# Kernel tuning notes

Measured on AMD Instinct MI355X. Metric: run time of the kernel, lower is better.

The kernel has to match this reference:

```python
import jax, jax.numpy as jnp
import numpy as np

Nn, Nt, Np, Ne = 100000, 30000, 400000, 1000000
IN_NODE, IN_NET, IN_PIN, IN_EDGE = 16, 8, 8, 4
H, HP, HE, L, T = 64, 16, 8, 3, 4
LOG2 = 0.6931471805599453  # ShiftedSoftplus shift


def _lrelu(x):
    return jax.nn.leaky_relu(x, 0.01)


def _ssp(x):  # DGL ShiftedSoftplus: softplus(x) - log(2)
    return jax.nn.softplus(x) - LOG2


def _forward(in_node_feat, in_net_feat, in_pin_feat, in_edge_feat,
             pins_src, pins_dst, near_src, near_dst,
             node_lin_W, node_lin_b, net_lin_W, net_lin_b,
             pin_lin_W, pin_lin_b, edge_lin_W, edge_lin_b,
             geom_W, geom_b, pins_W, pins_b,
             cf_node_W, cf_node_b, cf_e1_W, cf_e1_b, cf_e2_W, cf_e2_b,
             cf_out_W, cf_out_b, sage_pool_W, sage_pool_b,
             sage_self_W, sage_neigh_W, sage_bias,
             out1_W, out1_b, out2_W, out2_b, out3_W, out3_b,
             outn1_W, outn1_b, outn2_W, outn2_b, outn3_W, outn3_b):
    node_feat = _lrelu(in_node_feat @ node_lin_W + node_lin_b)   # [Nn,H]
    net_feat = _lrelu(in_net_feat @ net_lin_W + net_lin_b)       # [Nt,H]
    pin_feat = _lrelu(in_pin_feat @ pin_lin_W + pin_lin_b)       # [Np,HP]
    edge_feat = _lrelu(in_edge_feat @ edge_lin_W + edge_lin_b)   # [Ne,HE]

    # static degree norms for GraphConv(norm='both') on 'pins' (node->net)
    ones_p = jnp.ones((Np,), jnp.float32)
    deg_out = jax.ops.segment_sum(ones_p, pins_src, num_segments=Nn)
    deg_in = jax.ops.segment_sum(ones_p, pins_dst, num_segments=Nt)
    src_norm = jnp.clip(deg_out, 1.0, None) ** -0.5
    dst_norm = jnp.clip(deg_in, 1.0, None) ** -0.5

    for i in range(L):
        # --- 'pins' GraphConv (node -> net), norm='both' ---
        msg = (node_feat * src_norm[:, None])[pins_src]                 # [Np,H]
        agg = jax.ops.segment_sum(msg, pins_dst, num_segments=Nt)      # [Nt,H]
        net_out = (agg * dst_norm[:, None]) @ pins_W[i] + pins_b[i]

        # --- 'pinned' CFConv (net -> node), reverse pins, edge feats = pin_feat ---
        hv = net_feat @ cf_node_W[i] + cf_node_b[i]                    # [Nt,H]
        he = _ssp(pin_feat @ cf_e1_W[i] + cf_e1_b[i])
        he = _ssp(he @ cf_e2_W[i] + cf_e2_b[i])                        # [Np,H]
        m = hv[pins_dst] * he                                          # src of 'pinned' = pins_dst
        h_cf = jax.ops.segment_sum(m, pins_src, num_segments=Nn)       # dst of 'pinned' = pins_src
        node_cf = _ssp(h_cf @ cf_out_W[i] + cf_out_b[i])

        # --- 'near' SAGEConv(pool) with sigmoid edge weights ---
        ew = jax.nn.sigmoid(edge_feat @ geom_W[i] + geom_b[i])         # [Ne,1]
        hp = jax.nn.relu(node_feat @ sage_pool_W[i] + sage_pool_b[i])  # [Nn,H]
        m2 = hp[near_src] * ew                                         # [Ne,H], nonnegative
        h_neigh = jax.ops.segment_max(m2, near_dst, num_segments=Nn)
        h_neigh = jnp.maximum(h_neigh, 0.0)  # zero-degree nodes -> 0 (msgs are >= 0)
        node_sage = node_feat @ sage_self_W[i] + h_neigh @ sage_neigh_W[i] + sage_bias[i]

        # hetero max-aggregation over edge types hitting dst 'node'
        node_feat = _lrelu(jnp.maximum(node_cf, node_sage))
        net_feat = _lrelu(net_out)

    h = _lrelu(jnp.concatenate([in_node_feat, node_feat], axis=-1) @ out1_W + out1_b)
    h = _lrelu(h @ out2_W + out2_b)
    node_pred = jax.nn.sigmoid(h @ out3_W + out3_b)
    g = _lrelu(jnp.concatenate([in_net_feat, net_feat], axis=-1) @ outn1_W + outn1_b)
    g = _lrelu(g @ outn2_W + outn2_b)
    net_pred = jax.nn.sigmoid(g @ outn3_W + outn3_b)
    return node_pred, net_pred


def setup_inputs() -> dict:
    key = jax.random.key(0)
    ks = iter(jax.random.split(key, 80))

    def nrm(shape, scale=0.05):
        return jax.random.normal(next(ks), shape, jnp.float32) * scale

    inp = {}
    inp['in_node_feat'] = nrm((Nn, IN_NODE), 1.0)
    inp['in_net_feat'] = nrm((Nt, IN_NET), 1.0)
    inp['in_pin_feat'] = nrm((Np, IN_PIN), 1.0)
    inp['in_edge_feat'] = nrm((Ne, IN_EDGE), 1.0)
    inp['pins_src'] = jax.random.randint(next(ks), (Np,), 0, Nn)
    inp['pins_dst'] = jax.random.randint(next(ks), (Np,), 0, Nt)
    inp['near_src'] = jax.random.randint(next(ks), (Ne,), 0, Nn)
    inp['near_dst'] = jax.random.randint(next(ks), (Ne,), 0, Nn)
    inp['node_lin_W'] = nrm((IN_NODE, H)); inp['node_lin_b'] = nrm((H,))
    inp['net_lin_W'] = nrm((IN_NET, H)); inp['net_lin_b'] = nrm((H,))
    inp['pin_lin_W'] = nrm((IN_PIN, HP)); inp['pin_lin_b'] = nrm((HP,))
    inp['edge_lin_W'] = nrm((IN_EDGE, HE)); inp['edge_lin_b'] = nrm((HE,))
    inp['geom_W'] = nrm((L, HE, 1)); inp['geom_b'] = nrm((L, 1))
    inp['pins_W'] = nrm((L, H, H)); inp['pins_b'] = nrm((L, H))
    inp['cf_node_W'] = nrm((L, H, H)); inp['cf_node_b'] = nrm((L, H))
    inp['cf_e1_W'] = nrm((L, HP, H)); inp['cf_e1_b'] = nrm((L, H))
    inp['cf_e2_W'] = nrm((L, H, H)); inp['cf_e2_b'] = nrm((L, H))
    inp['cf_out_W'] = nrm((L, H, H)); inp['cf_out_b'] = nrm((L, H))
    inp['sage_pool_W'] = nrm((L, H, H)); inp['sage_pool_b'] = nrm((L, H))
    inp['sage_self_W'] = nrm((L, H, H))
    inp['sage_neigh_W'] = nrm((L, H, H))
    inp['sage_bias'] = nrm((L, H))
    inp['out1_W'] = nrm((IN_NODE + H, H)); inp['out1_b'] = nrm((H,))
    inp['out2_W'] = nrm((H, H)); inp['out2_b'] = nrm((H,))
    inp['out3_W'] = nrm((H, T)); inp['out3_b'] = nrm((T,))
    inp['outn1_W'] = nrm((IN_NET + H, H)); inp['outn1_b'] = nrm((H,))
    inp['outn2_W'] = nrm((H, H)); inp['outn2_b'] = nrm((H,))
    inp['outn3_W'] = nrm((H, 1)); inp['outn3_b'] = nrm((1,))
    return inp


def reference(in_node_feat, in_net_feat, in_pin_feat, in_edge_feat,
              pins_src, pins_dst, near_src, near_dst,
              node_lin_W, node_lin_b, net_lin_W, net_lin_b,
              pin_lin_W, pin_lin_b, edge_lin_W, edge_lin_b,
              geom_W, geom_b, pins_W, pins_b,
              cf_node_W, cf_node_b, cf_e1_W, cf_e1_b, cf_e2_W, cf_e2_b,
              cf_out_W, cf_out_b, sage_pool_W, sage_pool_b,
              sage_self_W, sage_neigh_W, sage_bias,
              out1_W, out1_b, out2_W, out2_b, out3_W, out3_b,
              outn1_W, outn1_b, outn2_W, outn2_b, outn3_W, outn3_b):
    return _forward(in_node_feat, in_net_feat, in_pin_feat, in_edge_feat,
                    pins_src, pins_dst, near_src, near_dst,
                    node_lin_W, node_lin_b, net_lin_W, net_lin_b,
                    pin_lin_W, pin_lin_b, edge_lin_W, edge_lin_b,
                    geom_W, geom_b, pins_W, pins_b,
                    cf_node_W, cf_node_b, cf_e1_W, cf_e1_b, cf_e2_W, cf_e2_b,
                    cf_out_W, cf_out_b, sage_pool_W, sage_pool_b,
                    sage_self_W, sage_neigh_W, sage_bias,
                    out1_W, out1_b, out2_W, out2_b, out3_W, out3_b,
                    outn1_W, outn1_b, outn2_W, outn2_b, outn3_W, outn3_b)
```

## Files before the change

kernel.cpp:

```cpp
#include <hip/hip_runtime.h>
#include <hip/hip_bf16.h>

#define DEV __device__ __forceinline__

DEV float lrelu_(float x){ return x > 0.f ? x : 0.01f * x; }
DEV float ssp_(float x){ return fmaxf(x, 0.f) + __logf(1.f + __expf(-fabsf(x))) - 0.69314718055994530942f; }
DEV float sigm_(float x){ return 1.f / (1.f + __expf(-x)); }

DEV unsigned short f2bf(float x){
    unsigned int u = __float_as_uint(x);
    unsigned int r = (u + 0x7FFFu + ((u >> 16) & 1u)) >> 16;
    return (unsigned short)r;
}
DEV float bf2f(unsigned short s){ return __uint_as_float((unsigned int)s << 16); }
DEV ushort4 pack4(float4 v){
    ushort4 u; u.x = f2bf(v.x); u.y = f2bf(v.y); u.z = f2bf(v.z); u.w = f2bf(v.w); return u;
}

DEV void fma44(float (&acc)[4][4], const float4 (&xa)[4], const float4 (&wa)[4])
{
    #pragma unroll
    for (int kk = 0; kk < 4; kk++) {
        #pragma unroll
        for (int i = 0; i < 4; i++) {
            float x = ((const float*)&xa[i])[kk];
            #pragma unroll
            for (int j = 0; j < 4; j++)
                acc[i][j] += x * ((const float*)&wa[kk])[j];
        }
    }
}

typedef short s8v __attribute__((ext_vector_type(8)));
typedef float f4v __attribute__((ext_vector_type(4)));

template<int K, int ACT, bool OUTBF>
__global__ __launch_bounds__(256) void gemm64_kernel(const float* __restrict__ X,
                                                     const float* __restrict__ W,
                                                     const float* __restrict__ B,
                                                     void* __restrict__ Yv, int nrows)
{
    constexpr int XS = K + 4;
    constexpr int KQ = K / 4;
    __shared__ float Ws[K * 64];
    __shared__ float bs[64];
    __shared__ float Xs[64 * XS];
    for (int i = threadIdx.x; i < K * 64; i += 256) Ws[i] = W[i];
    if (threadIdx.x < 64) bs[threadIdx.x] = B[threadIdx.x];
    const int tr = threadIdx.x >> 4, tc = threadIdx.x & 15;
    const int r0 = tr * 4, c0 = tc * 4;
    for (int base = blockIdx.x * 64; base < nrows; base += gridDim.x * 64) {
        __syncthreads();
        for (int i = threadIdx.x; i < 64 * KQ; i += 256) {
            int row = i / KQ, kq = (i % KQ) * 4;
            int g = base + row;
            float4 v = make_float4(0.f, 0.f, 0.f, 0.f);
            if (g < nrows) v = *(const float4*)&X[(size_t)g * K + kq];
            *(float4*)&Xs[row * XS + kq] = v;
        }
        __syncthreads();
        float acc[4][4];
        #pragma unroll
        for (int i = 0; i < 4; i++)
            #pragma unroll
            for (int j = 0; j < 4; j++) acc[i][j] = bs[c0 + j];
        #pragma unroll 4
        for (int kq = 0; kq < K; kq += 4) {
            float4 xa[4], wa[4];
            #pragma unroll
            for (int i = 0; i < 4; i++) xa[i] = *(const float4*)&Xs[(r0 + i) * XS + kq];
            #pragma unroll
            for (int j = 0; j < 4; j++) wa[j] = *(const float4*)&Ws[(kq + j) * 64 + c0];
            fma44(acc, xa, wa);
        }
        #pragma unroll
        for (int i = 0; i < 4; i++) {
            int g = base + r0 + i;
            if (g < nrows) {
                float4 o;
                float* op = (float*)&o;
                #pragma unroll
                for (int j = 0; j < 4; j++) {
                    float a = acc[i][j];
                    if (ACT == 1) a = lrelu_(a);
                    else if (ACT == 2) a = fmaxf(a, 0.f);
                    op[j] = a;
                }
                if (OUTBF) *(ushort4*)&((unsigned short*)Yv)[(size_t)g * 64 + c0] = pack4(o);
                else       *(float4*)&((float*)Yv)[(size_t)g * 64 + c0] = o;
            }
        }
    }
}

template<int ACT, bool INBF, bool OUTBF>
__global__ __launch_bounds__(256) void mfma_gemm_kernel(const void* __restrict__ Xv,
                                                        const float* __restrict__ W,
                                                        const float* __restrict__ B,
                                                        void* __restrict__ Yv, int nrows)
{
    __shared__ __align__(16) unsigned short WT[64 * 72];
    __shared__ __align__(16) unsigned short Axs[64 * 72];
    __shared__ float bs[64];
    for (int i = threadIdx.x; i < 4096; i += 256) {
        int k = i >> 6, nn = i & 63;
        WT[nn * 72 + k] = f2bf(W[i]);
    }
    if (threadIdx.x < 64) bs[threadIdx.x] = B[threadIdx.x];
    const int lane = threadIdx.x & 63, wv = threadIdx.x >> 6;
    const int l15 = lane & 15, quad = lane >> 4;
    const int arow = 16 * wv + l15;
    const int koff = quad * 8;
    for (int base = blockIdx.x * 64; base < nrows; base += gridDim.x * 64) {
        __syncthreads();
        {
            int row = threadIdx.x >> 2, kq = (threadIdx.x & 3) * 16;
            int g = base + row;
            if (INBF) {
                const unsigned short* Xb = (const unsigned short*)Xv;
                uint4 v0 = make_uint4(0,0,0,0), v1 = v0;
                if (g < nrows) {
                    v0 = *(const uint4*)&Xb[(size_t)g * 64 + kq];
                    v1 = *(const uint4*)&Xb[(size_t)g * 64 + kq + 8];
                }
                *(uint4*)&Axs[row * 72 + kq] = v0;
                *(uint4*)&Axs[row * 72 + kq + 8] = v1;
            } else {
                const float* Xf = (const float*)Xv;
                #pragma unroll
                for (int m = 0; m < 4; m++) {
                    float4 v = make_float4(0,0,0,0);
                    if (g < nrows) v = *(const float4*)&Xf[(size_t)g * 64 + kq + m * 4];
                    *(ushort4*)&Axs[row * 72 + kq + m * 4] = pack4(v);
                }
            }
        }
        __syncthreads();
        f4v acc[4];
        #pragma unroll
        for (int t = 0; t < 4; t++) acc[t] = (f4v){0.f,0.f,0.f,0.f};
        s8v a0 = *(const s8v*)&Axs[arow * 72 + koff];
        s8v a1 = *(const s8v*)&Axs[arow * 72 + 32 + koff];
        #pragma unroll
        for (int t = 0; t < 4; t++) {
            int nn = t * 16 + l15;
            s8v b0 = *(const s8v*)&WT[nn * 72 + koff];
            s8v b1 = *(const s8v*)&WT[nn * 72 + 32 + koff];
            acc[t] = __builtin_amdgcn_mfma_f32_16x16x32_bf16(a0, b0, acc[t], 0, 0, 0);
            acc[t] = __builtin_amdgcn_mfma_f32_16x16x32_bf16(a1, b1, acc[t], 0, 0, 0);
        }
        const int mrow = 16 * wv + quad * 4;
        #pragma unroll
        for (int t = 0; t < 4; t++) {
            int col = t * 16 + l15;
            float b = bs[col];
            #pragma unroll
            for (int r = 0; r < 4; r++) {
                int g = base + mrow + r;
                if (g < nrows) {
                    float a = acc[t][r] + b;
                    if (ACT == 1) a = lrelu_(a);
                    else if (ACT == 2) a = fmaxf(a, 0.f);
                    if (OUTBF) ((unsigned short*)Yv)[(size_t)g * 64 + col] = f2bf(a);
                    else       ((float*)Yv)[(size_t)g * 64 + col] = a;
                }
            }
        }
    }
}

__global__ __launch_bounds__(256) void mfma_combine_kernel(const unsigned short* __restrict__ cfb,
                                                           const unsigned short* __restrict__ nfb,
                                                           const unsigned short* __restrict__ ngb,
                                                           const float* __restrict__ Wc, const float* __restrict__ cB,
                                                           const float* __restrict__ sW, const float* __restrict__ nW,
                                                           const float* __restrict__ sB,
                                                           unsigned short* __restrict__ outb, int n)
{
    __shared__ __align__(16) unsigned short WcT[64 * 72], WsT[64 * 72], WnT[64 * 72];
    __shared__ __align__(16) unsigned short Ac[32 * 72], As[32 * 72], An[32 * 72];
    __shared__ float bc[64], bsg[64];
    for (int i = threadIdx.x; i < 4096; i += 256) {
        int k = i >> 6, nn = i & 63;
        WcT[nn * 72 + k] = f2bf(Wc[i]);
        WsT[nn * 72 + k] = f2bf(sW[i]);
        WnT[nn * 72 + k] = f2bf(nW[i]);
    }
    if (threadIdx.x < 64) { bc[threadIdx.x] = cB[threadIdx.x]; bsg[threadIdx.x] = sB[threadIdx.x]; }
    const int lane = threadIdx.x & 63, wv = threadIdx.x >> 6;
    const int l15 = lane & 15, quad = lane >> 4;
    const int arow = (wv & 1) * 16 + l15;
    const int ct0 = (wv >> 1) * 2;
    const int koff = quad * 8;
    for (int base = blockIdx.x * 32; base < n; base += gridDim.x * 32) {
        __syncthreads();
        {
            int row = threadIdx.x >> 3, kq = (threadIdx.x & 7) * 8;
            int g = base + row;
            uint4 vc = make_uint4(0,0,0,0), vf = vc, vg = vc;
            if (g < n) {
                vc = *(const uint4*)&cfb[(size_t)g * 64 + kq];
                vf = *(const uint4*)&nfb[(size_t)g * 64 + kq];
                vg = *(const uint4*)&ngb[(size_t)g * 64 + kq];
            }
            *(uint4*)&Ac[row * 72 + kq] = vc;
            *(uint4*)&As[row * 72 + kq] = vf;
            *(uint4*)&An[row * 72 + kq] = vg;
        }
        __syncthreads();
        f4v accC[2], accS[2];
        #pragma unroll
        for (int t = 0; t < 2; t++) { accC[t] = (f4v){0.f,0.f,0.f,0.f}; accS[t] = (f4v){0.f,0.f,0.f,0.f}; }
        s8v ac0 = *(const s8v*)&Ac[arow * 72 + koff];
        s8v ac1 = *(const s8v*)&Ac[arow * 72 + 32 + koff];
        s8v as0 = *(const s8v*)&As[arow * 72 + koff];
        s8v as1 = *(const s8v*)&As[arow * 72 + 32 + koff];
        s8v an0 = *(const s8v*)&An[arow * 72 + koff];
        s8v an1 = *(const s8v*)&An[arow * 72 + 32 + koff];
        #pragma unroll
        for (int t = 0; t < 2; t++) {
            int nn = (ct0 + t) * 16 + l15;
            s8v wc0 = *(const s8v*)&WcT[nn * 72 + koff];
            s8v wc1 = *(const s8v*)&WcT[nn * 72 + 32 + koff];
            accC[t] = __builtin_amdgcn_mfma_f32_16x16x32_bf16(ac0, wc0, accC[t], 0, 0, 0);
            accC[t] = __builtin_amdgcn_mfma_f32_16x16x32_bf16(ac1, wc1, accC[t], 0, 0, 0);
            s8v ws0 = *(const s8v*)&WsT[nn * 72 + koff];
            s8v ws1 = *(const s8v*)&WsT[nn * 72 + 32 + koff];
            accS[t] = __builtin_amdgcn_mfma_f32_16x16x32_bf16(as0, ws0, accS[t], 0, 0, 0);
            accS[t] = __builtin_amdgcn_mfma_f32_16x16x32_bf16(as1, ws1, accS[t], 0, 0, 0);
            s8v wn0 = *(const s8v*)&WnT[nn * 72 + koff];
            s8v wn1 = *(const s8v*)&WnT[nn * 72 + 32 + koff];
            accS[t] = __builtin_amdgcn_mfma_f32_16x16x32_bf16(an0, wn0, accS[t], 0, 0, 0);
            accS[t] = __builtin_amdgcn_mfma_f32_16x16x32_bf16(an1, wn1, accS[t], 0, 0, 0);
        }
        const int mrow = (wv & 1) * 16 + quad * 4;
        #pragma unroll
        for (int t = 0; t < 2; t++) {
            int col = (ct0 + t) * 16 + l15;
            float bcv = bc[col], bsv = bsg[col];
            #pragma unroll
            for (int r = 0; r < 4; r++) {
                int g = base + mrow + r;
                if (g < n)
                    outb[(size_t)g * 64 + col] = f2bf(lrelu_(fmaxf(ssp_(accC[t][r] + bcv), accS[t][r] + bsv)));
            }
        }
    }
}

template<int K, int C, int ACT, bool OUTBF>
__global__ __launch_bounds__(256) void lin_kernel(const float* __restrict__ X,
                                                  const float* __restrict__ W,
                                                  const float* __restrict__ B,
                                                  void* __restrict__ Yv, int nrows)
{
    constexpr int ROWS = 256 / C;
    __shared__ float Ws[K * C];
    __shared__ float bs[C];
    __shared__ float Xs[ROWS * K];
    for (int i = threadIdx.x; i < K * C; i += 256) Ws[i] = W[i];
    if (threadIdx.x < C) bs[threadIdx.x] = B[threadIdx.x];
    __syncthreads();
    const int r = threadIdx.x / C, c = threadIdx.x % C;
    for (int base = blockIdx.x * ROWS; base < nrows; base += gridDim.x * ROWS) {
        __syncthreads();
        for (int i = threadIdx.x; i < ROWS * K; i += 256) {
            int rr = base + i / K;
            Xs[i] = (rr < nrows) ? X[(size_t)rr * K + i % K] : 0.f;
        }
        __syncthreads();
        int row = base + r;
        if (row < nrows) {
            float acc = bs[c];
            #pragma unroll
            for (int k = 0; k < K; k++) acc += Xs[r * K + k] * Ws[k * C + c];
            if (ACT == 1) acc = lrelu_(acc);
            else if (ACT == 2) acc = fmaxf(acc, 0.f);
            if (OUTBF) ((unsigned short*)Yv)[(size_t)row * C + c] = f2bf(acc);
            else       ((float*)Yv)[(size_t)row * C + c] = acc;
        }
    }
}

__global__ __launch_bounds__(256) void deg_kernel(const int* __restrict__ src, const int* __restrict__ dst,
                                                  int* __restrict__ cnt_src, int* __restrict__ cnt_dst, int np)
{
    int p = blockIdx.x * 256 + threadIdx.x;
    if (p < np) { atomicAdd(&cnt_src[src[p]], 1); atomicAdd(&cnt_dst[dst[p]], 1); }
}

__global__ __launch_bounds__(256) void norm_out_kernel(const int* __restrict__ cnt, float* __restrict__ out, int n)
{
    int i = blockIdx.x * 256 + threadIdx.x;
    if (i < n) {
        int v = cnt[i]; if (v < 1) v = 1;
        out[i] = rsqrtf((float)v);
    }
}

__global__ __launch_bounds__(256) void csr_count_kernel(const int* __restrict__ key, int* __restrict__ cnt, int ne)
{
    int e = blockIdx.x * 256 + threadIdx.x;
    if (e < ne) atomicAdd(&cnt[key[e]], 1);
}

__global__ __launch_bounds__(256) void scan_block_sum_kernel(const int* __restrict__ cnt, int* __restrict__ bsum, int n)
{
    __shared__ int sh[256];
    int i = blockIdx.x * 256 + threadIdx.x;
    sh[threadIdx.x] = (i < n) ? cnt[i] : 0;
    __syncthreads();
    for (int s = 128; s > 0; s >>= 1) {
        if (threadIdx.x < s) sh[threadIdx.x] += sh[threadIdx.x + s];
        __syncthreads();
    }
    if (threadIdx.x == 0) bsum[blockIdx.x] = sh[0];
}

__global__ __launch_bounds__(512) void scan_bsum_kernel(int* __restrict__ bsum, int nb, int* __restrict__ total_out)
{
    __shared__ int sh[512];
    int i = threadIdx.x;
    int v = (i < nb) ? bsum[i] : 0;
    sh[i] = v;
    __syncthreads();
    for (int s = 1; s < 512; s <<= 1) {
        int add = (i >= s) ? sh[i - s] : 0;
        __syncthreads();
        sh[i] += add;
        __syncthreads();
    }
    if (i < nb) bsum[i] = sh[i] - v;
    if (i == nb - 1) *total_out = sh[i];
}

__global__ __launch_bounds__(256) void scan_final_kernel(const int* __restrict__ cnt, const int* __restrict__ bsum,
                                                         int* __restrict__ row_start, int* __restrict__ nxt, int n)
{
    __shared__ int sh[256];
    int i = blockIdx.x * 256 + threadIdx.x;
    int v = (i < n) ? cnt[i] : 0;
    sh[threadIdx.x] = v;
    __syncthreads();
    for (int s = 1; s < 256; s <<= 1) {
        int add = (threadIdx.x >= s) ? sh[threadIdx.x - s] : 0;
        __syncthreads();
        sh[threadIdx.x] += add;
        __syncthreads();
    }
    if (i < n) {
        int excl = sh[threadIdx.x] - v + bsum[blockIdx.x];
        row_start[i] = excl;
        nxt[i] = excl;
    }
}

__global__ __launch_bounds__(256) void csr_fill_kernel(const int* __restrict__ key, int* __restrict__ nxt,
                                                       int* __restrict__ eidx, int ne, int nrows)
{
    const int color = blockIdx.x & 7;
    const int bid = blockIdx.x >> 3;
    const int nblk = gridDim.x >> 3;
    const int lo = (int)(((long long)nrows * color) >> 3);
    const int hi = (int)(((long long)nrows * (color + 1)) >> 3);
    for (int e = bid * 256 + threadIdx.x; e < ne; e += nblk * 256) {
        int k = key[e];
        if (k >= lo && k < hi) {
            int slot = atomicAdd(&nxt[k], 1);
            eidx[slot] = e;
        }
    }
}

__global__ __launch_bounds__(256) void pin_permute_kernel(const int* __restrict__ seidx,
                                                          const unsigned short* __restrict__ pinb,
                                                          const int* __restrict__ pdst,
                                                          unsigned short* __restrict__ pinb_s,
                                                          int* __restrict__ pdst_s, int np)
{
    int slot = blockIdx.x * 256 + threadIdx.x;
    if (slot < np) {
        int p = seidx[slot];
        uint4 a = *(const uint4*)&pinb[(size_t)p * 16];
        uint4 b = *(const uint4*)&pinb[(size_t)p * 16 + 8];
        *(uint4*)&pinb_s[(size_t)slot * 16] = a;
        *(uint4*)&pinb_s[(size_t)slot * 16 + 8] = b;
        pdst_s[slot] = pdst[p];
    }
}

__global__ __launch_bounds__(256) void pins_meta_permute_kernel(const int* __restrict__ peidx,
                                                                const int* __restrict__ psrc,
                                                                const float* __restrict__ snorm,
                                                                int* __restrict__ psrc_s,
                                                                float* __restrict__ snorm_s, int np)
{
    int slot = blockIdx.x * 256 + threadIdx.x;
    if (slot < np) {
        int s = psrc[peidx[slot]];
        psrc_s[slot] = s;
        snorm_s[slot] = snorm[s];
    }
}

__global__ __launch_bounds__(256) void near_meta_permute_kernel(const int* __restrict__ eidx,
                                                                const int* __restrict__ esrc,
                                                                int* __restrict__ esrc_s, int ne)
{
    int slot = blockIdx.x * 256 + threadIdx.x;
    if (slot < ne) esrc_s[slot] = esrc[eidx[slot]];
}

__global__ __launch_bounds__(256) void edge_ew_kernel(const float* __restrict__ in_edge,
                                                      const float* __restrict__ elW, const float* __restrict__ elb,
                                                      const float* __restrict__ gW, const float* __restrict__ gb,
                                                      float* __restrict__ ew3, int ne)
{
    __shared__ float W[32], B[8], G[24], Gb[3];
    if (threadIdx.x < 32) W[threadIdx.x] = elW[threadIdx.x];
    if (threadIdx.x < 8)  B[threadIdx.x] = elb[threadIdx.x];
    if (threadIdx.x < 24) G[threadIdx.x] = gW[threadIdx.x];
    if (threadIdx.x < 3)  Gb[threadIdx.x] = gb[threadIdx.x];
    __syncthreads();
    for (int e = blockIdx.x * 256 + threadIdx.x; e < ne; e += gridDim.x * 256) {
        float4 x = *(const float4*)&in_edge[(size_t)e * 4];
        float ef[8];
        #pragma unroll
        for (int j = 0; j < 8; j++)
            ef[j] = lrelu_(B[j] + x.x * W[j] + x.y * W[8 + j] + x.z * W[16 + j] + x.w * W[24 + j]);
        #pragma unroll
        for (int i = 0; i < 3; i++) {
            float a = Gb[i];
            #pragma unroll
            for (int j = 0; j < 8; j++) a += ef[j] * G[i * 8 + j];
            ew3[(size_t)i * ne + e] = sigm_(a);
        }
    }
}

__global__ __launch_bounds__(256) void pins_gather_kernel(const unsigned short* __restrict__ nfb,
                                                          const float* __restrict__ dnorm,
                                                          const int* __restrict__ psrc_s,
                                                          const float* __restrict__ snorm_s,
                                                          const int* __restrict__ prow,
                                                          unsigned short* __restrict__ aggb, int nt)
{
    __shared__ int sS[4][64];
    __shared__ float sN[4][64];
    const int lane = threadIdx.x & 63, wv = threadIdx.x >> 6;
    for (int d = blockIdx.x * 4 + wv; d < nt; d += gridDim.x * 4) {
        int rs = prow[d], re = prow[d + 1];
        float acc = 0.f;
        for (int cbase = rs; cbase < re; cbase += 64) {
            int cnt = re - cbase; if (cnt > 64) cnt = 64;
            if (lane < cnt) {
                sS[wv][lane] = psrc_s[cbase + lane];
                sN[wv][lane] = snorm_s[cbase + lane];
            }
            int k = 0;
            for (; k + 7 < cnt; k += 8) {
                float v[8];
                #pragma unroll
                for (int j = 0; j < 8; j++)
                    v[j] = bf2f(nfb[(size_t)sS[wv][k + j] * 64 + lane]) * sN[wv][k + j];
                acc += ((v[0] + v[1]) + (v[2] + v[3])) + ((v[4] + v[5]) + (v[6] + v[7]));
            }
            for (; k + 3 < cnt; k += 4) {
                float v0 = bf2f(nfb[(size_t)sS[wv][k]   * 64 + lane]) * sN[wv][k];
                float v1 = bf2f(nfb[(size_t)sS[wv][k+1] * 64 + lane]) * sN[wv][k+1];
                float v2 = bf2f(nfb[(size_t)sS[wv][k+2] * 64 + lane]) * sN[wv][k+2];
                float v3 = bf2f(nfb[(size_t)sS[wv][k+3] * 64 + lane]) * sN[wv][k+3];
                acc += (v0 + v1) + (v2 + v3);
            }
            for (; k < cnt; k++)
                acc += bf2f(nfb[(size_t)sS[wv][k] * 64 + lane]) * sN[wv][k];
        }
        aggb[(size_t)d * 64 + lane] = f2bf(acc * dnorm[d]);
    }
}

__global__ __launch_bounds__(256) void cf_pin6_kernel(const unsigned short* __restrict__ pinb,
                                                      const float* __restrict__ W1, const float* __restrict__ B1,
                                                      const float* __restrict__ W2, const float* __restrict__ B2,
                                                      unsigned short* __restrict__ HEb, int np)
{
    __shared__ __align__(16) unsigned short W1T[64 * 40];
    __shared__ __align__(16) unsigned short W2T[64 * 72];
    __shared__ __align__(16) unsigned short PFb[64 * 40];
    __shared__ __align__(16) unsigned short T1s[64 * 72];
    __shared__ float bs1[64], bs2[64];
    for (int i = threadIdx.x; i < 64 * 32; i += 256) {
        int n = i & 63, k = i >> 6;
        W1T[n * 40 + k] = (k < 16) ? f2bf(W1[k * 64 + n]) : (unsigned short)0;
    }
    for (int i = threadIdx.x; i < 4096; i += 256) {
        int k = i >> 6, n = i & 63;
        W2T[n * 72 + k] = f2bf(W2[i]);
    }
    if (threadIdx.x < 64) { bs1[threadIdx.x] = B1[threadIdx.x]; bs2[threadIdx.x] = B2[threadIdx.x]; }
    const int lane = threadIdx.x & 63, wv = threadIdx.x >> 6;
    const int l15 = lane & 15, quad = lane >> 4;
    const int arow = 16 * wv + l15;
    const int koff = quad * 8;
    const int mrow = 16 * wv + quad * 4;
    for (int base = blockIdx.x * 64; base < np; base += gridDim.x * 64) {
        __syncthreads();
        {
            int row = threadIdx.x >> 2, q = threadIdx.x & 3;
            int p = base + row;
            uint2 v = make_uint2(0, 0);
            if (p < np) v = *(const uint2*)&pinb[(size_t)p * 16 + q * 4];
            *(uint2*)&PFb[row * 40 + q * 4] = v;
            if (q < 2)
                *(uint4*)&PFb[row * 40 + 16 + q * 8] = make_uint4(0,0,0,0);
        }
        __syncthreads();
        {
            f4v acc1[4];
            #pragma unroll
            for (int t = 0; t < 4; t++) acc1[t] = (f4v){0.f,0.f,0.f,0.f};
            s8v a = *(const s8v*)&PFb[arow * 40 + koff];
            #pragma unroll
            for (int t = 0; t < 4; t++) {
                int n = t * 16 + l15;
                s8v b = *(const s8v*)&W1T[n * 40 + koff];
                acc1[t] = __builtin_amdgcn_mfma_f32_16x16x32_bf16(a, b, acc1[t], 0, 0, 0);
            }
            #pragma unroll
            for (int t = 0; t < 4; t++) {
                int col = t * 16 + l15;
                float b = bs1[col];
                #pragma unroll
                for (int r = 0; r < 4; r++)
                    T1s[(mrow + r) * 72 + col] = f2bf(ssp_(acc1[t][r] + b));
            }
        }
        __syncthreads();
        {
            f4v acc4[4];
            #pragma unroll
            for (int t = 0; t < 4; t++) acc4[t] = (f4v){0.f, 0.f, 0.f, 0.f};
            s8v a0 = *(const s8v*)&T1s[arow * 72 + koff];
            s8v a1 = *(const s8v*)&T1s[arow * 72 + 32 + koff];
            #pragma unroll
            for (int t = 0; t < 4; t++) {
                int n = t * 16 + l15;
                s8v b0 = *(const s8v*)&W2T[n * 72 + koff];
                s8v b1 = *(const s8v*)&W2T[n * 72 + 32 + koff];
                acc4[t] = __builtin_amdgcn_mfma_f32_16x16x32_bf16(a0, b0, acc4[t], 0, 0, 0);
                acc4[t] = __builtin_amdgcn_mfma_f32_16x16x32_bf16(a1, b1, acc4[t], 0, 0, 0);
            }
            __syncthreads();
            #pragma unroll
            for (int t = 0; t < 4; t++) {
                int col = t * 16 + l15;
                float b = bs2[col];
                #pragma unroll
                for (int r = 0; r < 4; r++)
                    T1s[(mrow + r) * 72 + col] = f2bf(ssp_(acc4[t][r] + b));
            }
        }
        __syncthreads();
        {
            int row = threadIdx.x >> 2, kq = (threadIdx.x & 3) * 16;
            int p = base + row;
            if (p < np) {
                *(uint4*)&HEb[(size_t)p * 64 + kq]     = *(const uint4*)&T1s[row * 72 + kq];
                *(uint4*)&HEb[(size_t)p * 64 + kq + 8] = *(const uint4*)&T1s[row * 72 + kq + 8];
            }
        }
    }
}

__global__ __launch_bounds__(256) void cf_gather_kernel(const unsigned short* __restrict__ HEb,
                                                        const unsigned short* __restrict__ hvb,
                                                        const int* __restrict__ pdst_s,
                                                        const int* __restrict__ srow,
                                                        unsigned short* __restrict__ cfb, int nn)
{
    __shared__ int sD[4][64];
    const int lane = threadIdx.x & 63, wv = threadIdx.x >> 6;
    for (int d = blockIdx.x * 4 + wv; d < nn; d += gridDim.x * 4) {
        int rs = srow[d], re = srow[d + 1];
        float acc = 0.f;
        for (int cbase = rs; cbase < re; cbase += 64) {
            int cnt = re - cbase; if (cnt > 64) cnt = 64;
            if (lane < cnt) {
                sD[wv][lane] = pdst_s[cbase + lane];
            }
            int k = 0;
            for (; k + 3 < cnt; k += 4) {
                float he[4], hv[4];
                #pragma unroll
                for (int j = 0; j < 4; j++) {
                    he[j] = bf2f(HEb[(size_t)(cbase + k + j) * 64 + lane]);
                    hv[j] = bf2f(hvb[(size_t)sD[wv][k + j] * 64 + lane]);
                }
                acc += (he[0] * hv[0] + he[1] * hv[1]) + (he[2] * hv[2] + he[3] * hv[3]);
            }
            for (; k < cnt; k++) {
                acc += bf2f(HEb[(size_t)(cbase + k) * 64 + lane]) * bf2f(hvb[(size_t)sD[wv][k] * 64 + lane]);
            }
        }
        cfb[(size_t)d * 64 + lane] = f2bf(acc);
    }
}

__global__ __launch_bounds__(256) void sage_gather_kernel(const unsigned short* __restrict__ hpb,
                                                          const float* __restrict__ ew,
                                                          const int* __restrict__ esrc_s,
                                                          const int* __restrict__ row_start,
                                                          const int* __restrict__ eidx,
                                                          unsigned short* __restrict__ ngb, int nn)
{
    __shared__ int sS[4][64];
    __shared__ float sWt[4][64];
    const int lane = threadIdx.x & 63, wv = threadIdx.x >> 6;
    for (int d = blockIdx.x * 4 + wv; d < nn; d += gridDim.x * 4) {
        int rs = row_start[d], re = row_start[d + 1];
        float acc = 0.f;
        for (int cbase = rs; cbase < re; cbase += 64) {
            int cnt = re - cbase; if (cnt > 64) cnt = 64;
            if (lane < cnt) {
                sS[wv][lane] = esrc_s[cbase + lane];
                sWt[wv][lane] = ew[eidx[cbase + lane]];
            }
            int k = 0;
            for (; k + 7 < cnt; k += 8) {
                float v[8];
                #pragma unroll
                for (int j = 0; j < 8; j++)
                    v[j] = bf2f(hpb[(size_t)sS[wv][k + j] * 64 + lane]) * sWt[wv][k + j];
                float m0 = fmaxf(fmaxf(v[0], v[1]), fmaxf(v[2], v[3]));
                float m1 = fmaxf(fmaxf(v[4], v[5]), fmaxf(v[6], v[7]));
                acc = fmaxf(acc, fmaxf(m0, m1));
            }
            for (; k + 3 < cnt; k += 4) {
                float v0 = bf2f(hpb[(size_t)sS[wv][k]   * 64 + lane]) * sWt[wv][k];
                float v1 = bf2f(hpb[(size_t)sS[wv][k+1] * 64 + lane]) * sWt[wv][k+1];
                float v2 = bf2f(hpb[(size_t)sS[wv][k+2] * 64 + lane]) * sWt[wv][k+2];
                float v3 = bf2f(hpb[(size_t)sS[wv][k+3] * 64 + lane]) * sWt[wv][k+3];
                acc = fmaxf(acc, fmaxf(fmaxf(v0, v1), fmaxf(v2, v3)));
            }
            for (; k < cnt; k++)
                acc = fmaxf(acc, bf2f(hpb[(size_t)sS[wv][k] * 64 + lane]) * sWt[wv][k]);
        }
        ngb[(size_t)d * 64 + lane] = f2bf(acc);
    }
}

__global__ __launch_bounds__(256) void node_head_mfma_kernel(const float* __restrict__ in_node,
                                                             const unsigned short* __restrict__ nfb,
                                                             const float* __restrict__ W1, const float* __restrict__ B1,
                                                             const float* __restrict__ W2, const float* __restrict__ B2,
                                                             const float* __restrict__ W3, const float* __restrict__ B3,
                                                             float* __restrict__ out, int n)
{
    __shared__ __align__(16) unsigned short W1T[64 * 104];
    __shared__ __align__(16) unsigned short W2T[64 * 72];
    __shared__ __align__(16) unsigned short W3T[16 * 72];
    __shared__ __align__(16) unsigned short Xs[64 * 104];
    __shared__ __align__(16) unsigned short H1[64 * 72];
    __shared__ float bs1[64], bs2[64], bs3[4];
    for (int i = threadIdx.x; i < 64 * 96; i += 256) {
        int k = i >> 6, nn = i & 63;
        W1T[nn * 104 + k] = (k < 80) ? f2bf(W1[k * 64 + nn]) : (unsigned short)0;
    }
    for (int i = threadIdx.x; i < 4096; i += 256) {
        int k = i >> 6, nn = i & 63;
        W2T[nn * 72 + k] = f2bf(W2[i]);
    }
    for (int i = threadIdx.x; i < 1024; i += 256) {
        int k = i >> 4, c = i & 15;
        W3T[c * 72 + k] = (c < 4) ? f2bf(W3[k * 4 + c]) : (unsigned short)0;
    }
    if (threadIdx.x < 64) { bs1[threadIdx.x] = B1[threadIdx.x]; bs2[threadIdx.x] = B2[threadIdx.x]; }
    if (threadIdx.x < 4) bs3[threadIdx.x] = B3[threadIdx.x];
    const int lane = threadIdx.x & 63, wv = threadIdx.x >> 6;
    const int l15 = lane & 15, quad = lane >> 4;
    const int arow = 16 * wv + l15;
    const int koff = quad * 8;
    const int mrow = 16 * wv + quad * 4;
    unsigned short* H2 = Xs;
    for (int base = blockIdx.x * 64; base < n; base += gridDim.x * 64) {
        __syncthreads();
        {
            int row = threadIdx.x >> 2, q = threadIdx.x & 3;
            int g = base + row;
            float4 v = make_float4(0,0,0,0);
            if (g < n) v = *(const float4*)&in_node[(size_t)g * 16 + q * 4];
            *(ushort4*)&Xs[row * 104 + q * 4] = pack4(v);
            uint4 u0 = make_uint4(0,0,0,0), u1 = u0;
            if (g < n) {
                u0 = *(const uint4*)&nfb[(size_t)g * 64 + q * 16];
                u1 = *(const uint4*)&nfb[(size_t)g * 64 + q * 16 + 8];
            }
            *(uint4*)&Xs[row * 104 + 16 + q * 16] = u0;
            *(uint4*)&Xs[row * 104 + 16 + q * 16 + 8] = u1;
            ushort4 z; z.x = 0; z.y = 0; z.z = 0; z.w = 0;
            *(ushort4*)&Xs[row * 104 + 80 + q * 4] = z;
        }
        __syncthreads();
        {
            f4v acc[4];
            #pragma unroll
            for (int t = 0; t < 4; t++) acc[t] = (f4v){0.f,0.f,0.f,0.f};
            s8v a0 = *(const s8v*)&Xs[arow * 104 + koff];
            s8v a1 = *(const s8v*)&Xs[arow * 104 + 32 + koff];
            s8v a2 = *(const s8v*)&Xs[arow * 104 + 64 + koff];
            #pragma unroll
            for (int t = 0; t < 4; t++) {
                int nn = t * 16 + l15;
                s8v b0 = *(const s8v*)&W1T[nn * 104 + koff];
                s8v b1 = *(const s8v*)&W1T[nn * 104 + 32 + koff];
                s8v b2 = *(const s8v*)&W1T[nn * 104 + 64 + koff];
                acc[t] = __builtin_amdgcn_mfma_f32_16x16x32_bf16(a0, b0, acc[t], 0, 0, 0);
                acc[t] = __builtin_amdgcn_mfma_f32_16x16x32_bf16(a1, b1, acc[t], 0, 0, 0);
                acc[t] = __builtin_amdgcn_mfma_f32_16x16x32_bf16(a2, b2, acc[t], 0, 0, 0);
            }
            #pragma unroll
            for (int t = 0; t < 4; t++) {
                int col = t * 16 + l15;
                float b = bs1[col];
                #pragma unroll
                for (int r = 0; r < 4; r++)
                    H1[(mrow + r) * 72 + col] = f2bf(lrelu_(acc[t][r] + b));
            }
        }
        __syncthreads();
        {
            f4v acc[4];
            #pragma unroll
            for (int t = 0; t < 4; t++) acc[t] = (f4v){0.f,0.f,0.f,0.f};
            s8v a0 = *(const s8v*)&H1[arow * 72 + koff];
            s8v a1 = *(const s8v*)&H1[arow * 72 + 32 + koff];
            #pragma unroll
            for (int t = 0; t < 4; t++) {
                int nn = t * 16 + l15;
                s8v b0 = *(const s8v*)&W2T[nn * 72 + koff];
                s8v b1 = *(const s8v*)&W2T[nn * 72 + 32 + koff];
                acc[t] = __builtin_amdgcn_mfma_f32_16x16x32_bf16(a0, b0, acc[t], 0, 0, 0);
                acc[t] = __builtin_amdgcn_mfma_f32_16x16x32_bf16(a1, b1, acc[t], 0, 0, 0);
            }
            __syncthreads();
            #pragma unroll
            for (int t = 0; t < 4; t++) {
                int col = t * 16 + l15;
                float b = bs2[col];
                #pragma unroll
                for (int r = 0; r < 4; r++)
                    H2[(mrow + r) * 72 + col] = f2bf(lrelu_(acc[t][r] + b));
            }
        }
        __syncthreads();
        {
            f4v acc = (f4v){0.f,0.f,0.f,0.f};
            s8v a0 = *(const s8v*)&H2[arow * 72 + koff];
            s8v a1 = *(const s8v*)&H2[arow * 72 + 32 + koff];
            s8v b0 = *(const s8v*)&W3T[l15 * 72 + koff];
            s8v b1 = *(const s8v*)&W3T[l15 * 72 + 32 + koff];
            acc = __builtin_amdgcn_mfma_f32_16x16x32_bf16(a0, b0, acc, 0, 0, 0);
            acc = __builtin_amdgcn_mfma_f32_16x16x32_bf16(a1, b1, acc, 0, 0, 0);
            if (l15 < 4) {
                float b = bs3[l15];
                #pragma unroll
                for (int r = 0; r < 4; r++) {
                    int g = base + mrow + r;
                    if (g < n) out[(size_t)g * 4 + l15] = sigm_(acc[r] + b);
                }
            }
        }
    }
}

__global__ __launch_bounds__(256) void net_head_mfma_kernel(const float* __restrict__ in_net, const float* __restrict__ tf,
                                                            const float* __restrict__ W1, const float* __restrict__ B1,
                                                            const float* __restrict__ W2, const float* __restrict__ B2,
                                                            const float* __restrict__ W3, const float* __restrict__ B3,
                                                            float* __restrict__ out, int n)
{
    __shared__ __align__(16) unsigned short W1T[64 * 104];
    __shared__ __align__(16) unsigned short W2T[64 * 72];
    __shared__ __align__(16) unsigned short W3T[16 * 72];
    __shared__ __align__(16) unsigned short Xs[64 * 104];
    __shared__ __align__(16) unsigned short H1[64 * 72];
    __shared__ float bs1[64], bs2[64], bs3[1];
    for (int i = threadIdx.x; i < 64 * 96; i += 256) {
        int k = i >> 6, nn = i & 63;
        W1T[nn * 104 + k] = (k < 72) ? f2bf(W1[k * 64 + nn]) : (unsigned short)0;
    }
    for (int i = threadIdx.x; i < 4096; i += 256) {
        int k = i >> 6, nn = i & 63;
        W2T[nn * 72 + k] = f2bf(W2[i]);
    }
    for (int i = threadIdx.x; i < 1024; i += 256) {
        int k = i >> 4, c = i & 15;
        W3T[c * 72 + k] = (c == 0) ? f2bf(W3[k]) : (unsigned short)0;
    }
    if (threadIdx.x < 64) { bs1[threadIdx.x] = B1[threadIdx.x]; bs2[threadIdx.x] = B2[threadIdx.x]; }
    if (threadIdx.x == 0) bs3[0] = B3[0];
    const int lane = threadIdx.x & 63, wv = threadIdx.x >> 6;
    const int l15 = lane & 15, quad = lane >> 4;
    const int arow = 16 * wv + l15;
    const int koff = quad * 8;
    const int mrow = 16 * wv + quad * 4;
    unsigned short* H2 = Xs;
    for (int base = blockIdx.x * 64; base < n; base += gridDim.x * 64) {
        __syncthreads();
        {
            int row = threadIdx.x >> 2, q = threadIdx.x & 3;
            int g = base + row;
            if (q < 2) {
                float4 v = make_float4(0,0,0,0);
                if (g < n) v = *(const float4*)&in_net[(size_t)g * 8 + q * 4];
                *(ushort4*)&Xs[row * 104 + q * 4] = pack4(v);
            }
            #pragma unroll
            for (int m = 0; m < 4; m++) {
                float4 v = make_float4(0,0,0,0);
                if (g < n) v = *(const float4*)&tf[(size_t)g * 64 + q * 16 + m * 4];
                *(ushort4*)&Xs[row * 104 + 8 + q * 16 + m * 4] = pack4(v);
            }
            if (q < 3) {
                ushort4 z; z.x = 0; z.y = 0; z.z = 0; z.w = 0;
                *(ushort4*)&Xs[row * 104 + 72 + q * 8] = z;
                *(ushort4*)&Xs[row * 104 + 72 + q * 8 + 4] = z;
            }
        }
        __syncthreads();
        {
            f4v acc[4];
            #pragma unroll
            for (int t = 0; t < 4; t++) acc[t] = (f4v){0.f,0.f,0.f,0.f};
            s8v a0 = *(const s8v*)&Xs[arow * 104 + koff];
            s8v a1 = *(const s8v*)&Xs[arow * 104 + 32 + koff];
            s8v a2 = *(const s8v*)&Xs[arow * 104 + 64 + koff];
            #pragma unroll
            for (int t = 0; t < 4; t++) {
                int nn = t * 16 + l15;
                s8v b0 = *(const s8v*)&W1T[nn * 104 + koff];
                s8v b1 = *(const s8v*)&W1T[nn * 104 + 32 + koff];
                s8v b2 = *(const s8v*)&W1T[nn * 104 + 64 + koff];
                acc[t] = __builtin_amdgcn_mfma_f32_16x16x32_bf16(a0, b0, acc[t], 0, 0, 0);
                acc[t] = __builtin_amdgcn_mfma_f32_16x16x32_bf16(a1, b1, acc[t], 0, 0, 0);
                acc[t] = __builtin_amdgcn_mfma_f32_16x16x32_bf16(a2, b2, acc[t], 0, 0, 0);
            }
            #pragma unroll
            for (int t = 0; t < 4; t++) {
                int col = t * 16 + l15;
                float b = bs1[col];
                #pragma unroll
                for (int r = 0; r < 4; r++)
                    H1[(mrow + r) * 72 + col] = f2bf(lrelu_(acc[t][r] + b));
            }
        }
        __syncthreads();
        {
            f4v acc[4];
            #pragma unroll
            for (int t = 0; t < 4; t++) acc[t] = (f4v){0.f,0.f,0.f,0.f};
            s8v a0 = *(const s8v*)&H1[arow * 72 + koff];
            s8v a1 = *(const s8v*)&H1[arow * 72 + 32 + koff];
            #pragma unroll
            for (int t = 0; t < 4; t++) {
                int nn = t * 16 + l15;
                s8v b0 = *(const s8v*)&W2T[nn * 72 + koff];
                s8v b1 = *(const s8v*)&W2T[nn * 72 + 32 + koff];
                acc[t] = __builtin_amdgcn_mfma_f32_16x16x32_bf16(a0, b0, acc[t], 0, 0, 0);
                acc[t] = __builtin_amdgcn_mfma_f32_16x16x32_bf16(a1, b1, acc[t], 0, 0, 0);
            }
            __syncthreads();
            #pragma unroll
            for (int t = 0; t < 4; t++) {
                int col = t * 16 + l15;
                float b = bs2[col];
                #pragma unroll
                for (int r = 0; r < 4; r++)
                    H2[(mrow + r) * 72 + col] = f2bf(lrelu_(acc[t][r] + b));
            }
        }
        __syncthreads();
        {
            f4v acc = (f4v){0.f,0.f,0.f,0.f};
            s8v a0 = *(const s8v*)&H2[arow * 72 + koff];
            s8v a1 = *(const s8v*)&H2[arow * 72 + 32 + koff];
            s8v b0 = *(const s8v*)&W3T[l15 * 72 + koff];
            s8v b1 = *(const s8v*)&W3T[l15 * 72 + 32 + koff];
            acc = __builtin_amdgcn_mfma_f32_16x16x32_bf16(a0, b0, acc, 0, 0, 0);
            acc = __builtin_amdgcn_mfma_f32_16x16x32_bf16(a1, b1, acc, 0, 0, 0);
            if (l15 == 0) {
                float b = bs3[0];
                #pragma unroll
                for (int r = 0; r < 4; r++) {
                    int g = base + mrow + r;
                    if (g < n) out[g] = sigm_(acc[r] + b);
                }
            }
        }
    }
}

extern "C" void kernel_launch(void* const* d_in, const int* in_sizes, int n_in,
                              void* d_out, int out_size, void* d_ws, size_t ws_size,
                              hipStream_t stream)
{
    (void)in_sizes; (void)n_in; (void)out_size; (void)ws_size;
    constexpr int Nn = 100000, Nt = 30000, Np = 400000, Ne = 1000000;
    constexpr int H = 64, L = 3, T = 4;

    auto fpt = [&](int i){ return (const float*)d_in[i]; };
    auto ipt = [&](int i){ return (const int*)d_in[i]; };

    const float* in_node = fpt(0);
    const float* in_net  = fpt(1);
    const float* in_pin  = fpt(2);
    const float* in_edge = fpt(3);
    const int* psrc = ipt(4);
    const int* pdst = ipt(5);
    const int* esrc = ipt(6);
    const int* edst = ipt(7);

    float* ws = (float*)d_ws;
    size_t o = 0;
    auto alloc = [&](size_t nel){ float* p = ws + o; o += nel; return p; };
    unsigned short* node_a = (unsigned short*)alloc((size_t)Nn * 32);
    unsigned short* node_b = (unsigned short*)alloc((size_t)Nn * 32);
    unsigned short* aggb   = (unsigned short*)alloc((size_t)Nt * 32);
    unsigned short* hvb    = (unsigned short*)alloc((size_t)Nt * 32);
    unsigned short* hpb    = (unsigned short*)alloc((size_t)Nn * 32);
    unsigned short* ngb    = (unsigned short*)alloc((size_t)Nn * 32);
    unsigned short* HEb    = (unsigned short*)alloc((size_t)Np * 32);
    unsigned short* cfb    = (unsigned short*)alloc((size_t)Nn * 32);
    float* net_a  = alloc((size_t)Nt * H);
    float* net_b  = alloc((size_t)Nt * H);
    unsigned short* pinb   = (unsigned short*)alloc((size_t)Np * 8);
    unsigned short* pinb_s = (unsigned short*)alloc((size_t)Np * 8);
    float* ew3    = alloc((size_t)3 * Ne);
    float* snorm  = alloc((size_t)Nn);
    float* dnorm  = alloc((size_t)Nt);
    int* cnt       = (int*)alloc((size_t)Nn);
    int* ecnt      = (int*)alloc((size_t)Nn);
    int* row_start = (int*)alloc((size_t)Nn + 1);
    int* nxt       = (int*)alloc((size_t)Nn);
    int* eidx      = (int*)alloc((size_t)Ne);
    int* bsum      = (int*)alloc((size_t)512);
    int* pcnt      = (int*)alloc((size_t)Nt);
    int* prow      = (int*)alloc((size_t)Nt + 1);
    int* pnxt      = (int*)alloc((size_t)Nt);
    int* peidx     = (int*)alloc((size_t)Np);
    int* pbsum     = (int*)alloc((size_t)256);
    int* srow      = (int*)alloc((size_t)Nn + 1);
    int* seidx     = (int*)alloc((size_t)Np);
    int* pdst_s    = (int*)alloc((size_t)Np);
    int* psrc_s    = (int*)alloc((size_t)Np);
    float* snorm_s = alloc((size_t)Np);
    int* esrc_s    = (int*)alloc((size_t)Ne);

    constexpr int NB  = (Nn + 255) / 256;
    constexpr int NB2 = (Nt + 255) / 256;

    hipMemsetAsync(cnt, 0, (size_t)Nn * 4, stream);
    hipMemsetAsync(pcnt, 0, (size_t)Nt * 4, stream);
    deg_kernel<<<(Np + 255) / 256, 256, 0, stream>>>(psrc, pdst, cnt, pcnt, Np);
    norm_out_kernel<<<(Nn + 255) / 256, 256, 0, stream>>>(cnt, snorm, Nn);
    norm_out_kernel<<<(Nt + 255) / 256, 256, 0, stream>>>(pcnt, dnorm, Nt);

    hipMemsetAsync(ecnt, 0, (size_t)Nn * 4, stream);
    csr_count_kernel<<<(Ne + 255) / 256, 256, 0, stream>>>(edst, ecnt, Ne);
    scan_block_sum_kernel<<<NB, 256, 0, stream>>>(ecnt, bsum, Nn);
    scan_bsum_kernel<<<1, 512, 0, stream>>>(bsum, NB, row_start + Nn);
    scan_final_kernel<<<NB, 256, 0, stream>>>(ecnt, bsum, row_start, nxt, Nn);
    csr_fill_kernel<<<2048, 256, 0, stream>>>(edst, nxt, eidx, Ne, Nn);
    near_meta_permute_kernel<<<(Ne + 255) / 256, 256, 0, stream>>>(eidx, esrc, esrc_s, Ne);

    scan_block_sum_kernel<<<NB2, 256, 0, stream>>>(pcnt, pbsum, Nt);
    scan_bsum_kernel<<<1, 512, 0, stream>>>(pbsum, NB2, prow + Nt);
    scan_final_kernel<<<NB2, 256, 0, stream>>>(pcnt, pbsum, prow, pnxt, Nt);
    csr_fill_kernel<<<1024, 256, 0, stream>>>(pdst, pnxt, peidx, Np, Nt);
    pins_meta_permute_kernel<<<(Np + 255) / 256, 256, 0, stream>>>(peidx, psrc, snorm, psrc_s, snorm_s, Np);

    scan_block_sum_kernel<<<NB, 256, 0, stream>>>(cnt, bsum, Nn);
    scan_bsum_kernel<<<1, 512, 0, stream>>>(bsum, NB, srow + Nn);
    scan_final_kernel<<<NB, 256, 0, stream>>>(cnt, bsum, srow, nxt, Nn);
    csr_fill_kernel<<<1024, 256, 0, stream>>>(psrc, nxt, seidx, Np, Nn);

    gemm64_kernel<16, 1, true><<<1024, 256, 0, stream>>>(in_node, fpt(8),  fpt(9),  node_a, Nn);
    gemm64_kernel< 8, 1, false><<<469, 256, 0, stream>>>(in_net,  fpt(10), fpt(11), net_a,  Nt);
    lin_kernel<8, 16, 1, true><<<1024, 256, 0, stream>>>(in_pin, fpt(12), fpt(13), pinb, Np);
    edge_ew_kernel<<<2048, 256, 0, stream>>>(in_edge, fpt(14), fpt(15), fpt(16), fpt(17), ew3, Ne);

    pin_permute_kernel<<<(Np + 255) / 256, 256, 0, stream>>>(seidx, pinb, pdst, pinb_s, pdst_s, Np);

    unsigned short* ncur = node_a; unsigned short* nnew = node_b;
    float* tcur = net_a;  float* tnew = net_b;

    for (int i = 0; i < L; i++) {
        pins_gather_kernel<<<(Nt + 3) / 4, 256, 0, stream>>>(ncur, dnorm, psrc_s, snorm_s, prow, aggb, Nt);
        mfma_gemm_kernel<1, true, false><<<469, 256, 0, stream>>>(aggb, fpt(18) + (size_t)i * 4096, fpt(19) + (size_t)i * 64, tnew, Nt);

        mfma_gemm_kernel<0, false, true><<<469, 256, 0, stream>>>(tcur, fpt(20) + (size_t)i * 4096, fpt(21) + (size_t)i * 64, hvb, Nt);
        cf_pin6_kernel<<<1024, 256, 0, stream>>>(pinb_s,
                                                 fpt(22) + (size_t)i * 1024, fpt(23) + (size_t)i * 64,
                                                 fpt(24) + (size_t)i * 4096, fpt(25) + (size_t)i * 64,
                                                 HEb, Np);
        cf_gather_kernel<<<(Nn + 3) / 4, 256, 0, stream>>>(HEb, hvb, pdst_s, srow, cfb, Nn);

        mfma_gemm_kernel<2, true, true><<<1024, 256, 0, stream>>>(ncur, fpt(28) + (size_t)i * 4096, fpt(29) + (size_t)i * 64, hpb, Nn);
        sage_gather_kernel<<<(Nn + 3) / 4, 256, 0, stream>>>(hpb, ew3 + (size_t)i * Ne, esrc_s, row_start, eidx, ngb, Nn);

        mfma_combine_kernel<<<1024, 256, 0, stream>>>(cfb, ncur, ngb,
                                                      fpt(26) + (size_t)i * 4096, fpt(27) + (size_t)i * 64,
                                                      fpt(30) + (size_t)i * 4096, fpt(31) + (size_t)i * 4096,
                                                      fpt(32) + (size_t)i * 64,
                                                      nnew, Nn);

        unsigned short* t = ncur; ncur = nnew; nnew = t;
        float* tf = tcur; tcur = tnew; tnew = tf;
    }

    float* out = (float*)d_out;
    node_head_mfma_kernel<<<784, 256, 0, stream>>>(in_node, ncur, fpt(33), fpt(34), fpt(35), fpt(36), fpt(37), fpt(38), out, Nn);
    net_head_mfma_kernel<<<469, 256, 0, stream>>>(in_net, tcur, fpt(39), fpt(40), fpt(41), fpt(42), fpt(43), fpt(44), out + (size_t)Nn * T, Nt);
}
```

Measured before the change: 960.9 us.

## Fuse CFConv edge MLP with segmented atomic scatter into node buffer

Folds the CFConv message and aggregation into the pin edge-MLP kernel. Each wave walks its 16 source-sorted pins, multiplies the on-chip he tile by the gathered hv row, and adds run-segmented partial sums into an fp32 node buffer with atomics. This removes the HEb round-trip through global memory and the separate gather kernel. In exchange it adds a per-layer memset and fp32 atomics, and the combine kernel now reads fp32 values and converts them to bf16. Summation order is no longer deterministic.

```diff
diff --git a/kernel.cpp b/kernel.cpp
--- a/kernel.cpp
+++ b/kernel.cpp
@@ -169,7 +169,7 @@
     }
 }
 
-__global__ __launch_bounds__(256) void mfma_combine_kernel(const unsigned short* __restrict__ cfb,
+__global__ __launch_bounds__(256) void mfma_combine_kernel(const float* __restrict__ cff,
                                                            const unsigned short* __restrict__ nfb,
                                                            const unsigned short* __restrict__ ngb,
                                                            const float* __restrict__ Wc, const float* __restrict__ cB,
@@ -197,13 +197,16 @@
         {
             int row = threadIdx.x >> 3, kq = (threadIdx.x & 7) * 8;
             int g = base + row;
-            uint4 vc = make_uint4(0,0,0,0), vf = vc, vg = vc;
+            uint4 vf = make_uint4(0,0,0,0), vg = vf;
+            float4 c0 = make_float4(0,0,0,0), c1 = c0;
             if (g < n) {
-                vc = *(const uint4*)&cfb[(size_t)g * 64 + kq];
+                c0 = *(const float4*)&cff[(size_t)g * 64 + kq];
+                c1 = *(const float4*)&cff[(size_t)g * 64 + kq + 4];
                 vf = *(const uint4*)&nfb[(size_t)g * 64 + kq];
                 vg = *(const uint4*)&ngb[(size_t)g * 64 + kq];
             }
-            *(uint4*)&Ac[row * 72 + kq] = vc;
+            *(ushort4*)&Ac[row * 72 + kq]     = pack4(c0);
+            *(ushort4*)&Ac[row * 72 + kq + 4] = pack4(c1);
             *(uint4*)&As[row * 72 + kq] = vf;
             *(uint4*)&An[row * 72 + kq] = vg;
         }
@@ -375,8 +378,10 @@
 __global__ __launch_bounds__(256) void pin_permute_kernel(const int* __restrict__ seidx,
                                                           const unsigned short* __restrict__ pinb,
                                                           const int* __restrict__ pdst,
+                                                          const int* __restrict__ psrc,
                                                           unsigned short* __restrict__ pinb_s,
-                                                          int* __restrict__ pdst_s, int np)
+                                                          int* __restrict__ pdst_s,
+                                                          int* __restrict__ snode_s, int np)
 {
     int slot = blockIdx.x * 256 + threadIdx.x;
     if (slot < np) {
@@ -386,6 +391,7 @@
         *(uint4*)&pinb_s[(size_t)slot * 16] = a;
         *(uint4*)&pinb_s[(size_t)slot * 16 + 8] = b;
         pdst_s[slot] = pdst[p];
+        snode_s[slot] = psrc[p];
     }
 }
 
@@ -479,10 +485,13 @@
     }
 }
 
-__global__ __launch_bounds__(256) void cf_pin6_kernel(const unsigned short* __restrict__ pinb,
-                                                      const float* __restrict__ W1, const float* __restrict__ B1,
-                                                      const float* __restrict__ W2, const float* __restrict__ B2,
-                                                      unsigned short* __restrict__ HEb, int np)
+__global__ __launch_bounds__(256) void cf_fused_kernel(const unsigned short* __restrict__ pinb,
+                                                       const float* __restrict__ W1, const float* __restrict__ B1,
+                                                       const float* __restrict__ W2, const float* __restrict__ B2,
+                                                       const unsigned short* __restrict__ hvb,
+                                                       const int* __restrict__ pdst_s,
+                                                       const int* __restrict__ snode_s,
+                                                       float* __restrict__ cff, int np)
 {
     __shared__ __align__(16) unsigned short W1T[64 * 40];
     __shared__ __align__(16) unsigned short W2T[64 * 72];
@@ -562,47 +571,27 @@
         }
         __syncthreads();
         {
-            int row = threadIdx.x >> 2, kq = (threadIdx.x & 3) * 16;
-            int p = base + row;
-            if (p < np) {
-                *(uint4*)&HEb[(size_t)p * 64 + kq]     = *(const uint4*)&T1s[row * 72 + kq];
-                *(uint4*)&HEb[(size_t)p * 64 + kq + 8] = *(const uint4*)&T1s[row * 72 + kq + 8];
-            }
-        }
-    }
-}
-
-__global__ __launch_bounds__(256) void cf_gather_kernel(const unsigned short* __restrict__ HEb,
-                                                        const unsigned short* __restrict__ hvb,
-                                                        const int* __restrict__ pdst_s,
-                                                        const int* __restrict__ srow,
-                                                        unsigned short* __restrict__ cfb, int nn)
-{
-    __shared__ int sD[4][64];
-    const int lane = threadIdx.x & 63, wv = threadIdx.x >> 6;
-    for (int d = blockIdx.x * 4 + wv; d < nn; d += gridDim.x * 4) {
-        int rs = srow[d], re = srow[d + 1];
-        float acc = 0.f;
-        for (int cbase = rs; cbase < re; cbase += 64) {
-            int cnt = re - cbase; if (cnt > 64) cnt = 64;
-            if (lane < cnt) {
-                sD[wv][lane] = pdst_s[cbase + lane];
-            }
-            int k = 0;
-            for (; k + 3 < cnt; k += 4) {
-                float he[4], hv[4];
-                #pragma unroll
-                for (int j = 0; j < 4; j++) {
-                    he[j] = bf2f(HEb[(size_t)(cbase + k + j) * 64 + lane]);
-                    hv[j] = bf2f(hvb[(size_t)sD[wv][k + j] * 64 + lane]);
+            int s0 = base + wv * 16;
+            if (s0 < np) {
+                int cur = snode_s[s0];
+                float acc = 0.f;
+                #pragma unroll 4
+                for (int k = 0; k < 16; k++) {
+                    int slot = s0 + k;
+                    if (slot >= np) break;
+                    int node = snode_s[slot];
+                    float he = bf2f(T1s[(wv * 16 + k) * 72 + lane]);
+                    float hv = bf2f(hvb[(size_t)pdst_s[slot] * 64 + lane]);
+                    if (node != cur) {
+                        atomicAdd(&cff[(size_t)cur * 64 + lane], acc);
+                        acc = 0.f;
+                        cur = node;
+                    }
+                    acc += he * hv;
                 }
-                acc += (he[0] * hv[0] + he[1] * hv[1]) + (he[2] * hv[2] + he[3] * hv[3]);
-            }
-            for (; k < cnt; k++) {
-                acc += bf2f(HEb[(size_t)(cbase + k) * 64 + lane]) * bf2f(hvb[(size_t)sD[wv][k] * 64 + lane]);
-            }
-        }
-        cfb[(size_t)d * 64 + lane] = f2bf(acc);
+                atomicAdd(&cff[(size_t)cur * 64 + lane], acc);
+            }
+        }
     }
 }
 
@@ -929,8 +918,7 @@
     unsigned short* hvb    = (unsigned short*)alloc((size_t)Nt * 32);
     unsigned short* hpb    = (unsigned short*)alloc((size_t)Nn * 32);
     unsigned short* ngb    = (unsigned short*)alloc((size_t)Nn * 32);
-    unsigned short* HEb    = (unsigned short*)alloc((size_t)Np * 32);
-    unsigned short* cfb    = (unsigned short*)alloc((size_t)Nn * 32);
+    float* cff   = alloc((size_t)Nn * 64);
     float* net_a  = alloc((size_t)Nt * H);
     float* net_b  = alloc((size_t)Nt * H);
     unsigned short* pinb   = (unsigned short*)alloc((size_t)Np * 8);
@@ -952,6 +940,7 @@
     int* srow      = (int*)alloc((size_t)Nn + 1);
     int* seidx     = (int*)alloc((size_t)Np);
     int* pdst_s    = (int*)alloc((size_t)Np);
+    int* snode_s   = (int*)alloc((size_t)Np);
     int* psrc_s    = (int*)alloc((size_t)Np);
     float* snorm_s = alloc((size_t)Np);
     int* esrc_s    = (int*)alloc((size_t)Ne);
@@ -989,7 +978,7 @@
     lin_kernel<8, 16, 1, true><<<1024, 256, 0, stream>>>(in_pin, fpt(12), fpt(13), pinb, Np);
     edge_ew_kernel<<<2048, 256, 0, stream>>>(in_edge, fpt(14), fpt(15), fpt(16), fpt(17), ew3, Ne);
 
-    pin_permute_kernel<<<(Np + 255) / 256, 256, 0, stream>>>(seidx, pinb, pdst, pinb_s, pdst_s, Np);
+    pin_permute_kernel<<<(Np + 255) / 256, 256, 0, stream>>>(seidx, pinb, pdst, psrc, pinb_s, pdst_s, snode_s, Np);
 
     unsigned short* ncur = node_a; unsigned short* nnew = node_b;
     float* tcur = net_a;  float* tnew = net_b;
@@ -999,16 +988,16 @@
         mfma_gemm_kernel<1, true, false><<<469, 256, 0, stream>>>(aggb, fpt(18) + (size_t)i * 4096, fpt(19) + (size_t)i * 64, tnew, Nt);
 
         mfma_gemm_kernel<0, false, true><<<469, 256, 0, stream>>>(tcur, fpt(20) + (size_t)i * 4096, fpt(21) + (size_t)i * 64, hvb, Nt);
-        cf_pin6_kernel<<<1024, 256, 0, stream>>>(pinb_s,
-                                                 fpt(22) + (size_t)i * 1024, fpt(23) + (size_t)i * 64,
-                                                 fpt(24) + (size_t)i * 4096, fpt(25) + (size_t)i * 64,
-                                                 HEb, Np);
-        cf_gather_kernel<<<(Nn + 3) / 4, 256, 0, stream>>>(HEb, hvb, pdst_s, srow, cfb, Nn);
+        hipMemsetAsync(cff, 0, (size_t)Nn * 64 * 4, stream);
+        cf_fused_kernel<<<1024, 256, 0, stream>>>(pinb_s,
+                                                  fpt(22) + (size_t)i * 1024, fpt(23) + (size_t)i * 64,
+                                                  fpt(24) + (size_t)i * 4096, fpt(25) + (size_t)i * 64,
+                                                  hvb, pdst_s, snode_s, cff, Np);
 
         mfma_gemm_kernel<2, true, true><<<1024, 256, 0, stream>>>(ncur, fpt(28) + (size_t)i * 4096, fpt(29) + (size_t)i * 64, hpb, Nn);
         sage_gather_kernel<<<(Nn + 3) / 4, 256, 0, stream>>>(hpb, ew3 + (size_t)i * Ne, esrc_s, row_start, eidx, ngb, Nn);
 
-        mfma_combine_kernel<<<1024, 256, 0, stream>>>(cfb, ncur, ngb,
+        mfma_combine_kernel<<<1024, 256, 0, stream>>>(cff, ncur, ngb,
                                                       fpt(26) + (size_t)i * 4096, fpt(27) + (size_t)i * 64,
                                                       fpt(30) + (size_t)i * 4096, fpt(31) + (size_t)i * 4096,
                                                       fpt(32) + (size_t)i * 64,
```

Result: slower. 1.025 ms (+6.6%).
